# Performance work log

Hardware: AMD Instinct MI355X
Metric: run time of the kernel (lower is better)

The kernel has to match this reference:

```python
import jax, jax.numpy as jnp
import numpy as np
import math

H = 1024      # hidden_size
NH = 16       # num_attention_heads
HD = H // NH  # head_dim = 64
FF = 4096     # intermediate_size
AD = 256      # adapter_hidden_size
NB = 320      # num_buckets
MAXD = 800    # max_bucket_distance
B = 4
S = 1024
EPS = 1e-5


def _rel_bucket(rel):
    # HF WavLM _relative_positions_bucket
    nb = NB // 2
    buckets = (rel > 0).astype(jnp.int32) * nb
    rel = jnp.abs(rel)
    max_exact = nb // 2
    is_small = rel < max_exact
    large = max_exact + (
        jnp.log(jnp.maximum(rel, 1).astype(jnp.float32) / max_exact)
        / math.log(MAXD / max_exact) * (nb - max_exact)
    ).astype(jnp.int32)
    large = jnp.minimum(large, nb - 1)
    return buckets + jnp.where(is_small, rel, large)


def _ln(x, g, b):
    m = x.mean(-1, keepdims=True)
    v = ((x - m) ** 2).mean(-1, keepdims=True)
    return (x - m) * jax.lax.rsqrt(v + EPS) * g + b


def setup_inputs() -> dict:
    key = jax.random.key(0)
    ks = jax.random.split(key, 12)
    sc = 0.02
    w = lambda k, shape: jax.random.normal(k, shape, jnp.float32) * sc
    return dict(
        x=jax.random.normal(ks[0], (B, S, H), jnp.float32),
        Wq=w(ks[1], (H, H)), bq=jnp.zeros((H,), jnp.float32),
        Wk=w(ks[2], (H, H)), bk=jnp.zeros((H,), jnp.float32),
        Wv=w(ks[3], (H, H)), bv=jnp.zeros((H,), jnp.float32),
        Wo=w(ks[4], (H, H)), bo=jnp.zeros((H,), jnp.float32),
        Wg=w(ks[5], (8, HD)), bg=jnp.zeros((8,), jnp.float32),
        gru_const=jnp.ones((1, NH, 1, 1), jnp.float32),
        rel_embed=w(ks[6], (NB, NH)),
        ln1_g=jnp.ones((H,), jnp.float32), ln1_b=jnp.zeros((H,), jnp.float32),
        W1=w(ks[7], (FF, H)), b1=jnp.zeros((FF,), jnp.float32),
        W2=w(ks[8], (H, FF)), b2=jnp.zeros((H,), jnp.float32),
        ln2_g=jnp.ones((H,), jnp.float32), ln2_b=jnp.zeros((H,), jnp.float32),
        Wad=w(ks[9], (AD, H)), bad=jnp.zeros((AD,), jnp.float32),
        Wau=w(ks[10], (H, AD)), bau=jnp.zeros((H,), jnp.float32),
    )


def reference(x, Wq, bq, Wk, bk, Wv, bv, Wo, bo, Wg, bg, gru_const, rel_embed,
              ln1_g, ln1_b, W1, b1, W2, b2, ln2_g, ln2_b, Wad, bad, Wau, bau):
    b, s, _ = x.shape
    # --- relative position bias (first layer: position_bias=None) ---
    pos = jnp.arange(s)
    rel = pos[None, :] - pos[:, None]                 # memory - context
    pos_bias = rel_embed[_rel_bucket(rel)].transpose(2, 0, 1)  # (nh, s, s)

    # --- GRU-style gating of the bias (per batch, head, query pos) ---
    xh = x.reshape(b, s, NH, HD).transpose(0, 2, 1, 3)         # (b, nh, s, hd)
    gproj = jnp.einsum('bhsd,ed->bhse', xh, Wg) + bg           # (b, nh, s, 8)
    gproj = gproj.reshape(b, NH, s, 2, 4).sum(-1)              # (b, nh, s, 2)
    gate = jax.nn.sigmoid(gproj)
    gate_a, gate_b = gate[..., 0:1], gate[..., 1:2]            # (b, nh, s, 1)
    gate_out = gate_a * (gate_b * gru_const - 1.0) + 2.0       # (b, nh, s, 1)
    gated_bias = gate_out * pos_bias[None]                     # (b, nh, s, s)

    # --- multi-head self-attention with additive gated bias ---
    q = (x @ Wq.T + bq).reshape(b, s, NH, HD)
    k = (x @ Wk.T + bk).reshape(b, s, NH, HD)
    v = (x @ Wv.T + bv).reshape(b, s, NH, HD)
    scores = jnp.einsum('bihd,bjhd->bhij', q, k) * (HD ** -0.5) + gated_bias
    attn = jax.nn.softmax(scores, axis=-1)
    ctx = jnp.einsum('bhij,bjhd->bihd', attn, v).reshape(b, s, H)
    attn_out = ctx @ Wo.T + bo

    # --- residual + LN, FFN + adapter (idx_without_adapter=None path) + LN ---
    h = _ln(x + attn_out, ln1_g, ln1_b)
    ff = jax.nn.gelu(h @ W1.T + b1, approximate=False) @ W2.T + b2
    adapt = jax.nn.elu(h @ Wad.T + bad) @ Wau.T + bau
    h = h + ff + adapt
    return _ln(h, ln2_g, ln2_b)
```

## Files before the change

### kernel.cpp

```cpp
#include <hip/hip_runtime.h>
#include <cmath>

typedef unsigned short u16;
using short8 = __attribute__((ext_vector_type(8))) short;
using f32x4  = __attribute__((ext_vector_type(4))) float;

__device__ __forceinline__ u16 f2bf(float f) {
  union { float f; unsigned u; } c; c.f = f;
  unsigned r = c.u + 0x7fffu + ((c.u >> 16) & 1u);
  return (u16)(r >> 16);
}
__device__ __forceinline__ float bf2f(u16 b) {
  union { unsigned u; float f; } c; c.u = ((unsigned)b) << 16;
  return c.f;
}

__device__ __forceinline__ void gld_lds16(void* lds, const void* g) {
  __builtin_amdgcn_global_load_lds(
      (const __attribute__((address_space(1))) void*)g,
      (__attribute__((address_space(3))) void*)lds, 16, 0, 0);
}

__device__ __forceinline__ float gelu_fast(float t) {
  float u = 0.7978845608f * t * (1.f + 0.044715f * t * t);
  float th = 1.f - 2.f / (__expf(2.f * u) + 1.f);
  return 0.5f * t * (1.f + th);
}

__global__ __launch_bounds__(256) void cvt_bf16(const float* __restrict__ in,
                                                u16* __restrict__ out, int n4) {
  int i = blockIdx.x * 256 + threadIdx.x;
  if (i >= n4) return;
  float4 v = ((const float4*)in)[i];
  ushort4 o;
  o.x = f2bf(v.x); o.y = f2bf(v.y); o.z = f2bf(v.z); o.w = f2bf(v.w);
  ((ushort4*)out)[i] = o;
}

__global__ __launch_bounds__(256) void cvt_pad(const float* __restrict__ in,
                                               u16* __restrict__ out,
                                               int incols4, int outstride, int n4) {
  int i = blockIdx.x * 256 + threadIdx.x;
  if (i >= n4) return;
  int row = i / incols4, c = i - row * incols4;
  float4 v = ((const float4*)in)[i];
  ushort4 o;
  o.x = f2bf(v.x); o.y = f2bf(v.y); o.z = f2bf(v.z); o.w = f2bf(v.w);
  *(ushort4*)&out[(size_t)row * outstride + c * 4] = o;
}

__global__ __launch_bounds__(256) void btab_kernel(const float* __restrict__ rel_embed,
                                                   float* __restrict__ btab) {
  int idx = blockIdx.x * 256 + threadIdx.x;
  if (idx >= 16 * 2048) return;
  int h = idx >> 11;
  int d = idx & 2047;
  if (d >= 2047) return;
  int rel = d - 1023;
  int bucket = (rel > 0) ? 160 : 0;
  int ar = rel < 0 ? -rel : rel;
  if (ar < 80) {
    bucket += ar;
  } else {
    int large = 80 + (int)(logf((float)ar / 80.0f) / 2.3025851f * 80.0f);
    if (large > 159) large = 159;
    bucket += large;
  }
  btab[h * 2048 + d] = rel_embed[bucket * 16 + h];
}

__global__ __launch_bounds__(256) void gate_kernel(const float* __restrict__ x,
                                                   const float* __restrict__ Wg,
                                                   const float* __restrict__ bg,
                                                   const float* __restrict__ gc,
                                                   float* __restrict__ gate_out) {
  int gw = blockIdx.x * 4 + (threadIdx.x >> 6);
  int lane = threadIdx.x & 63;
  int s = gw & 1023, bh = gw >> 10, b = bh >> 4, h = bh & 15;
  float wA = Wg[lane] + Wg[64 + lane] + Wg[128 + lane] + Wg[192 + lane];
  float wB = Wg[256 + lane] + Wg[320 + lane] + Wg[384 + lane] + Wg[448 + lane];
  float xv = x[((size_t)(b * 1024 + s)) * 1024 + h * 64 + lane];
  float pa = xv * wA, pb = xv * wB;
  #pragma unroll
  for (int m = 1; m < 64; m <<= 1) {
    pa += __shfl_xor(pa, m, 64);
    pb += __shfl_xor(pb, m, 64);
  }
  if (lane == 0) {
    float bgA = bg[0] + bg[1] + bg[2] + bg[3];
    float bgB = bg[4] + bg[5] + bg[6] + bg[7];
    float ga = 1.f / (1.f + expf(-(pa + bgA)));
    float gb = 1.f / (1.f + expf(-(pb + bgB)));
    gate_out[(size_t)bh * 1024 + s] = ga * (gb * gc[h] - 1.f) + 2.f;
  }
}

__global__ __launch_bounds__(256) void vtrans_kernel(const u16* __restrict__ vb,
                                                     u16* __restrict__ vt) {
  __shared__ u16 tile[64 * 65];
  int bh = blockIdx.y, b = bh >> 4, h = bh & 15;
  int s0 = blockIdx.x * 64;
  int tid = threadIdx.x;
  int r = tid >> 3, c = (tid & 7) * 8;
  #pragma unroll
  for (int p = 0; p < 2; ++p) {
    int s = p * 32 + r;
    uint4 vv = *(const uint4*)&vb[((size_t)(b * 1024 + s0 + s)) * 1024 + h * 64 + c];
    const u16* pv = (const u16*)&vv;
    #pragma unroll
    for (int e = 0; e < 8; ++e) tile[(c + e) * 65 + s] = pv[e];
  }
  __syncthreads();
  int d = tid & 63, jc0 = tid >> 6;
  #pragma unroll
  for (int jc = jc0; jc < 8; jc += 4) {
    u16 tmp[8];
    #pragma unroll
    for (int e = 0; e < 8; ++e) tmp[e] = tile[d * 65 + jc * 8 + e];
    *(uint4*)&vt[((size_t)(bh * 64 + d)) * 1024 + s0 + jc * 8] = *(uint4*)tmp;
  }
}

template <int MODE>
__global__ __launch_bounds__(256, 3) void gemm_bt(
    const u16* __restrict__ A, const u16* __restrict__ Bw,
    int K, int Ksub, int N,
    const float* __restrict__ bias0, const float* __restrict__ bias1,
    const float* __restrict__ bias2,
    float* __restrict__ outf,
    u16* __restrict__ ob0, u16* __restrict__ ob1, u16* __restrict__ ob2) {
  __shared__ __align__(16) u16 As[3][128 * 32];
  __shared__ __align__(16) u16 Bs[3][128 * 32];
  const int tid = threadIdx.x;
  const int lane = tid & 63, wave = tid >> 6;
  const int quad = lane >> 4, l16 = lane & 15;
  const int bm = blockIdx.x * 128, bn = blockIdx.y * 128;
  const int kz = blockIdx.z;
  const int nsteps = Ksub >> 5;
  const int wm = (wave & 1) * 64, wn = (wave >> 1) * 64;
  const int sr = lane & 15, skc = (lane >> 4) * 8;

  const u16* a0 = A + (size_t)(bm + wave * 32 + sr) * K + kz * Ksub + skc;
  const u16* b0 = Bw + (size_t)(bn + wave * 32 + sr) * K + kz * Ksub + skc;
  const size_t ra = (size_t)16 * K;

  f32x4 acc[4][4] = {};

  #pragma unroll
  for (int t = 0; t < 2; ++t) {
    gld_lds16(&As[0][(wave * 2 + t) * 512], a0 + t * ra);
    gld_lds16(&Bs[0][(wave * 2 + t) * 512], b0 + t * ra);
  }
  if (nsteps > 1) {
    #pragma unroll
    for (int t = 0; t < 2; ++t) {
      gld_lds16(&As[1][(wave * 2 + t) * 512], a0 + t * ra + 32);
      gld_lds16(&Bs[1][(wave * 2 + t) * 512], b0 + t * ra + 32);
    }
  }

  int cur = 0, nxt2 = 2;
  for (int ks = 0; ks < nsteps; ++ks) {
    if (ks + 1 < nsteps) asm volatile("s_waitcnt vmcnt(4)" ::: "memory");
    else                 asm volatile("s_waitcnt vmcnt(0)" ::: "memory");
    __builtin_amdgcn_s_barrier();
    if (ks + 2 < nsteps) {
      int ko = (ks + 2) * 32;
      #pragma unroll
      for (int t = 0; t < 2; ++t) {
        gld_lds16(&As[nxt2][(wave * 2 + t) * 512], a0 + t * ra + ko);
        gld_lds16(&Bs[nxt2][(wave * 2 + t) * 512], b0 + t * ra + ko);
      }
    }
    const u16* Ap = As[cur];
    const u16* Bp = Bs[cur];
    short8 af[4], bf[4];
    #pragma unroll
    for (int mi = 0; mi < 4; ++mi)
      af[mi] = *(const short8*)&Ap[((wm >> 4) + mi) * 512 + quad * 128 + l16 * 8];
    #pragma unroll
    for (int ni = 0; ni < 4; ++ni)
      bf[ni] = *(const short8*)&Bp[((wn >> 4) + ni) * 512 + quad * 128 + l16 * 8];
    #pragma unroll
    for (int mi = 0; mi < 4; ++mi)
      #pragma unroll
      for (int ni = 0; ni < 4; ++ni)
        acc[mi][ni] = __builtin_amdgcn_mfma_f32_16x16x32_bf16(af[mi], bf[ni], acc[mi][ni], 0, 0, 0);
    cur = (cur == 2) ? 0 : cur + 1;
    nxt2 = (nxt2 == 2) ? 0 : nxt2 + 1;
  }

  float* outp = outf + (size_t)kz * 4194304;

  #pragma unroll
  for (int mi = 0; mi < 4; ++mi) {
    #pragma unroll
    for (int ni = 0; ni < 4; ++ni) {
      int col = bn + wn + ni * 16 + l16;
      #pragma unroll
      for (int r = 0; r < 4; ++r) {
        int m = bm + wm + mi * 16 + quad * 4 + r;
        float v = acc[mi][ni][r];
        if constexpr (MODE == 0) {
          int seg = col >> 10;
          int nloc = col & 1023;
          const float* bs = seg == 0 ? bias0 : (seg == 1 ? bias1 : bias2);
          u16* dst = seg == 0 ? ob0 : (seg == 1 ? ob1 : ob2);
          v += bs[nloc];
          if (seg == 0) v *= 0.125f;
          dst[(size_t)m * 1024 + nloc] = f2bf(v);
        } else if constexpr (MODE == 2) {
          if (col < 4096) {
            float t = v + bias0[col];
            ob0[(size_t)m * 4352 + col] = f2bf(gelu_fast(t));
          } else {
            float t = v + bias1[col - 4096];
            float e = t > 0.f ? t : (__expf(t) - 1.f);
            ob0[(size_t)m * 4352 + col] = f2bf(e);
          }
        } else {
          outp[(size_t)m * N + col] = v;
        }
      }
    }
  }
}

__global__ __launch_bounds__(256) void attn_kernel(
    const u16* __restrict__ qb, const u16* __restrict__ kb, const u16* __restrict__ vt,
    const float* __restrict__ gate, const float* __restrict__ btab,
    u16* __restrict__ ctxb) {
  __shared__ __align__(16) u16 Qs[64 * 64];
  __shared__ __align__(16) u16 Ks[64 * 64];
  __shared__ __align__(16) u16 Vs[64 * 64];
  __shared__ __align__(16) u16 Ps[4][16 * 64];
  __shared__ u16 btl[2048];
  __shared__ float gbuf[64];

  const int tid = threadIdx.x;
  const int lane = tid & 63, wave = tid >> 6;
  const int quad = lane >> 4, l16 = lane & 15;
  const int it0 = blockIdx.x * 64;
  const int bh = blockIdx.y, b = bh >> 4, h = bh & 15;
  const int sr = lane & 15;
  const int skc = (lane >> 4) * 8;

  for (int idx = tid; idx < 2047; idx += 256) btl[idx] = f2bf(btab[h * 2048 + idx]);
  if (tid < 64) gbuf[tid] = gate[(size_t)bh * 1024 + it0 + tid];

  #pragma unroll
  for (int hf = 0; hf < 2; ++hf)
    gld_lds16(&Qs[wave * 1024 + hf * 512],
              &qb[((size_t)(b * 1024 + it0 + wave * 16 + sr)) * 1024 + h * 64 + hf * 32 + skc]);

  f32x4 oacc[4] = {};
  float mrow[4], lrow[4];
  #pragma unroll
  for (int r = 0; r < 4; ++r) { mrow[r] = -1e30f; lrow[r] = 0.f; }

  __syncthreads();

  for (int jt = 0; jt < 16; ++jt) {
    int j0 = jt * 64;
    #pragma unroll
    for (int hf = 0; hf < 2; ++hf) {
      gld_lds16(&Ks[wave * 1024 + hf * 512],
                &kb[((size_t)(b * 1024 + j0 + wave * 16 + sr)) * 1024 + h * 64 + hf * 32 + skc]);
      gld_lds16(&Vs[wave * 1024 + hf * 512],
                &vt[((size_t)(bh * 64 + wave * 16 + sr)) * 1024 + j0 + hf * 32 + skc]);
    }
    __syncthreads();

    f32x4 sacc[4] = {};
    #pragma unroll
    for (int c = 0; c < 2; ++c) {
      short8 aq = *(const short8*)&Qs[wave * 1024 + (c * 4 + quad) * 128 + l16 * 8];
      #pragma unroll
      for (int nt = 0; nt < 4; ++nt) {
        short8 bk8 = *(const short8*)&Ks[nt * 1024 + (c * 4 + quad) * 128 + l16 * 8];
        sacc[nt] = __builtin_amdgcn_mfma_f32_16x16x32_bf16(aq, bk8, sacc[nt], 0, 0, 0);
      }
    }

    float sc[4][4], mt[4];
    #pragma unroll
    for (int r = 0; r < 4; ++r) {
      int i_loc = wave * 16 + quad * 4 + r;
      int i_glob = it0 + i_loc;
      float g = gbuf[i_loc];
      float mx = -1e30f;
      #pragma unroll
      for (int nt = 0; nt < 4; ++nt) {
        int j = j0 + nt * 16 + l16;
        float s = sacc[nt][r] + g * bf2f(btl[j - i_glob + 1023]);
        sc[nt][r] = s;
        mx = fmaxf(mx, s);
      }
      mt[r] = mx;
    }
    #pragma unroll
    for (int m = 1; m < 16; m <<= 1)
      #pragma unroll
      for (int r = 0; r < 4; ++r) mt[r] = fmaxf(mt[r], __shfl_xor(mt[r], m, 64));

    float alpha[4], ls[4];
    #pragma unroll
    for (int r = 0; r < 4; ++r) {
      float mnew = fmaxf(mrow[r], mt[r]);
      alpha[r] = __expf(mrow[r] - mnew);
      mrow[r] = mnew;
      float lsum = 0.f;
      #pragma unroll
      for (int nt = 0; nt < 4; ++nt) {
        float p = __expf(sc[nt][r] - mnew);
        sc[nt][r] = p;
        lsum += p;
      }
      ls[r] = lsum;
    }
    #pragma unroll
    for (int m = 1; m < 16; m <<= 1)
      #pragma unroll
      for (int r = 0; r < 4; ++r) ls[r] += __shfl_xor(ls[r], m, 64);
    #pragma unroll
    for (int r = 0; r < 4; ++r) lrow[r] = lrow[r] * alpha[r] + ls[r];

    #pragma unroll
    for (int nt = 0; nt < 4; ++nt)
      #pragma unroll
      for (int r = 0; r < 4; ++r)
        Ps[wave][(nt * 2 + (l16 >> 3)) * 128 + (quad * 4 + r) * 8 + (l16 & 7)] = f2bf(sc[nt][r]);

    #pragma unroll
    for (int dt = 0; dt < 4; ++dt)
      #pragma unroll
      for (int r = 0; r < 4; ++r) oacc[dt][r] *= alpha[r];

    #pragma unroll
    for (int c = 0; c < 2; ++c) {
      short8 ap = *(const short8*)&Ps[wave][(c * 4 + quad) * 128 + l16 * 8];
      #pragma unroll
      for (int dt = 0; dt < 4; ++dt) {
        short8 bv8 = *(const short8*)&Vs[dt * 1024 + (c * 4 + quad) * 128 + l16 * 8];
        oacc[dt] = __builtin_amdgcn_mfma_f32_16x16x32_bf16(ap, bv8, oacc[dt], 0, 0, 0);
      }
    }
    __syncthreads();
  }

  #pragma unroll
  for (int dt = 0; dt < 4; ++dt)
    #pragma unroll
    for (int r = 0; r < 4; ++r) {
      int i_loc = wave * 16 + quad * 4 + r;
      int d = dt * 16 + l16;
      float o = oacc[dt][r] / lrow[r];
      ctxb[((size_t)(b * 1024 + it0 + i_loc)) * 1024 + h * 64 + d] = f2bf(o);
    }
}

template <bool WRITE_BF16, bool TWO_BIAS>
__global__ __launch_bounds__(256) void redln_kernel(
    const float* __restrict__ p0, const float* __restrict__ p1,
    const float* __restrict__ extra, const float* __restrict__ bias,
    const float* __restrict__ bias2,
    const float* __restrict__ g, const float* __restrict__ bta,
    float* __restrict__ outf, u16* __restrict__ outb) {
  __shared__ float red[8];
  int row = blockIdx.x, tid = threadIdx.x;
  int lane = tid & 63, wave = tid >> 6;
  size_t base = (size_t)row * 1024 + tid * 4;
  float4 a = *(const float4*)&p0[base];
  float4 bb = *(const float4*)&p1[base];
  float4 c = *(const float4*)&extra[base];
  float4 d = *(const float4*)&bias[tid * 4];
  float4 v;
  v.x = a.x + bb.x + c.x + d.x;
  v.y = a.y + bb.y + c.y + d.y;
  v.z = a.z + bb.z + c.z + d.z;
  v.w = a.w + bb.w + c.w + d.w;
  if (TWO_BIAS) {
    float4 d2 = *(const float4*)&bias2[tid * 4];
    v.x += d2.x; v.y += d2.y; v.z += d2.z; v.w += d2.w;
  }
  float s = v.x + v.y + v.z + v.w;
  #pragma unroll
  for (int m = 1; m < 64; m <<= 1) s += __shfl_xor(s, m, 64);
  if (lane == 0) red[wave] = s;
  __syncthreads();
  float mean = (red[0] + red[1] + red[2] + red[3]) * (1.f / 1024.f);
  float d0 = v.x - mean, d1 = v.y - mean, d2 = v.z - mean, d3 = v.w - mean;
  float sq = d0 * d0 + d1 * d1 + d2 * d2 + d3 * d3;
  #pragma unroll
  for (int m = 1; m < 64; m <<= 1) sq += __shfl_xor(sq, m, 64);
  if (lane == 0) red[4 + wave] = sq;
  __syncthreads();
  float var = (red[4] + red[5] + red[6] + red[7]) * (1.f / 1024.f);
  float rstd = rsqrtf(var + 1e-5f);
  float dd[4] = {d0, d1, d2, d3};
  #pragma unroll
  for (int e = 0; e < 4; ++e) {
    int cidx = tid * 4 + e;
    float val = dd[e] * rstd * g[cidx] + bta[cidx];
    outf[(size_t)row * 1024 + cidx] = val;
    if (WRITE_BF16) outb[(size_t)row * 1024 + cidx] = f2bf(val);
  }
}

extern "C" void kernel_launch(void* const* d_in, const int* in_sizes, int n_in,
                              void* d_out, int out_size, void* d_ws, size_t ws_size,
                              hipStream_t stream) {
  const float* x    = (const float*)d_in[0];
  const float* Wq   = (const float*)d_in[1];  const float* bq  = (const float*)d_in[2];
  const float* Wk   = (const float*)d_in[3];  const float* bk  = (const float*)d_in[4];
  const float* Wv   = (const float*)d_in[5];  const float* bv  = (const float*)d_in[6];
  const float* Wo   = (const float*)d_in[7];  const float* bo  = (const float*)d_in[8];
  const float* Wg   = (const float*)d_in[9];  const float* bg  = (const float*)d_in[10];
  const float* gc   = (const float*)d_in[11];
  const float* rel  = (const float*)d_in[12];
  const float* ln1g = (const float*)d_in[13]; const float* ln1b = (const float*)d_in[14];
  const float* W1   = (const float*)d_in[15]; const float* b1  = (const float*)d_in[16];
  const float* W2   = (const float*)d_in[17]; const float* b2  = (const float*)d_in[18];
  const float* ln2g = (const float*)d_in[19]; const float* ln2b = (const float*)d_in[20];
  const float* Wad  = (const float*)d_in[21]; const float* bad = (const float*)d_in[22];
  const float* Wau  = (const float*)d_in[23]; const float* bau = (const float*)d_in[24];
  float* out = (float*)d_out;

  char* ws = (char*)d_ws;
  const size_t MB = 1ull << 20;
  const size_t KB = 1ull << 10;
  u16*   xb    = (u16*)(ws + 0 * MB);
  u16*   wqkv  = (u16*)(ws + 8 * MB);
  u16*   qb    = (u16*)(ws + 14 * MB);
  u16*   kb    = (u16*)(ws + 22 * MB);
  u16*   vbp   = (u16*)(ws + 30 * MB);
  u16*   vtb   = (u16*)(ws + 38 * MB);
  float* gate  = (float*)(ws + 46 * MB);
  float* btab  = (float*)(ws + 46 * MB + 256 * KB);
  u16*   ffadp = (u16*)(ws + 0 * MB);
  float* P0    = (float*)(ws + 34 * MB);
  float* P1    = (float*)(ws + 50 * MB);
  u16*   ctxb  = (u16*)(ws + 66 * MB);
  u16*   wob   = (u16*)(ws + 74 * MB);
  u16*   w1ad  = (u16*)(ws + 76 * MB);
  u16*   w2au  = (u16*)(ws + 85 * MB);
  float* hf    = (float*)(ws + 94 * MB);
  u16*   hb    = (u16*)(ws + 110 * MB);
  (void)ws_size; (void)n_in; (void)in_sizes; (void)out_size;

  auto cvt = [&](const float* src, u16* dst, int n) {
    cvt_bf16<<<(n / 4 + 255) / 256, 256, 0, stream>>>(src, dst, n / 4);
  };
  cvt(x, xb, 4096 * 1024);
  cvt(Wq, wqkv,               1024 * 1024);
  cvt(Wk, wqkv + 1024 * 1024, 1024 * 1024);
  cvt(Wv, wqkv + 2 * 1024 * 1024, 1024 * 1024);
  cvt(Wo, wob, 1024 * 1024);
  cvt(W1, w1ad, 4096 * 1024);
  cvt(Wad, w1ad + 4096 * 1024, 256 * 1024);
  cvt_pad<<<(1024 * 1024 + 255) / 256, 256, 0, stream>>>(W2, w2au, 1024, 4352, 1024 * 1024);
  cvt_pad<<<(64 * 1024 + 255) / 256, 256, 0, stream>>>(Wau, w2au + 4096, 64, 4352, 64 * 1024);

  btab_kernel<<<128, 256, 0, stream>>>(rel, btab);
  gate_kernel<<<16384, 256, 0, stream>>>(x, Wg, bg, gc, gate);

  gemm_bt<0><<<dim3(32, 24, 1), 256, 0, stream>>>(xb, wqkv, 1024, 1024, 3072,
      bq, bk, bv, nullptr, qb, kb, vbp);
  vtrans_kernel<<<dim3(16, 64), 256, 0, stream>>>(vbp, vtb);
  attn_kernel<<<dim3(16, 64), 256, 0, stream>>>(qb, kb, vtb, gate, btab, ctxb);
  gemm_bt<3><<<dim3(32, 8, 2), 256, 0, stream>>>(ctxb, wob, 1024, 512, 1024,
      nullptr, nullptr, nullptr, P0, nullptr, nullptr, nullptr);
  redln_kernel<true, false><<<4096, 256, 0, stream>>>(P0, P1, x, bo, nullptr,
      ln1g, ln1b, hf, hb);
  gemm_bt<2><<<dim3(32, 34, 1), 256, 0, stream>>>(hb, w1ad, 1024, 1024, 4352,
      b1, bad, nullptr, nullptr, ffadp, nullptr, nullptr);
  gemm_bt<3><<<dim3(32, 8, 2), 256, 0, stream>>>(ffadp, w2au, 4352, 2176, 1024,
      nullptr, nullptr, nullptr, P0, nullptr, nullptr, nullptr);
  redln_kernel<false, true><<<4096, 256, 0, stream>>>(P0, P1, hf, b2, bau,
      ln2g, ln2b, out, nullptr);
}
```

Measured before the change: 538.6 us.

## Add 256x256 double-buffered GEMM kernel with 8-wave pipelining for large projections

Adds a new 512-thread GEMM kernel that computes 256x256 tiles, loads into LDS directly from global memory with swizzled offsets, uses phased barriers with set-priority around the MFMA blocks, and remaps block indices for locality. It replaces the QKV, FFN-up and FFN-down GEMMs. The adapter slice of FFN-up moves to a small launch of the old kernel using a new column offset. When the workspace is large enough, the workspace is laid out again and FFN-down uses a 4-way K split with a 4-input reduce+LN. The larger tiles mean fewer blocks, which risks leaving CUs idle on small grids such as 16x4x2.

```diff
diff --git a/kernel.cpp b/kernel.cpp
--- a/kernel.cpp
+++ b/kernel.cpp
@@ -124,7 +124,7 @@
 template <int MODE>
 __global__ __launch_bounds__(256, 3) void gemm_bt(
     const u16* __restrict__ A, const u16* __restrict__ Bw,
-    int K, int Ksub, int N,
+    int K, int Ksub, int N, int bn0,
     const float* __restrict__ bias0, const float* __restrict__ bias1,
     const float* __restrict__ bias2,
     float* __restrict__ outf,
@@ -196,7 +196,7 @@
   for (int mi = 0; mi < 4; ++mi) {
     #pragma unroll
     for (int ni = 0; ni < 4; ++ni) {
-      int col = bn + wn + ni * 16 + l16;
+      int col = bn + bn0 + wn + ni * 16 + l16;
       #pragma unroll
       for (int r = 0; r < 4; ++r) {
         int m = bm + wm + mi * 16 + quad * 4 + r;
@@ -226,6 +226,170 @@
   }
 }
 
+#define VMCNT(n) asm volatile("s_waitcnt vmcnt(" #n ")" ::: "memory")
+#define NOOPST ((void)0)
+
+#define G256_LDA(BUF, KK, MH)                                               \
+  af_[0] = *(const short8*)&lds[BUF][0][KK][aBase + (MH) * 2048 + 0];       \
+  af_[1] = *(const short8*)&lds[BUF][0][KK][aBase + (MH) * 2048 + 512];     \
+  af_[2] = *(const short8*)&lds[BUF][0][KK][aBase + (MH) * 2048 + 1024];    \
+  af_[3] = *(const short8*)&lds[BUF][0][KK][aBase + (MH) * 2048 + 1536];
+#define G256_LDB(BUF, KK)                                                   \
+  bf_[0] = *(const short8*)&lds[BUF][1][KK][bBase + 0];                     \
+  bf_[1] = *(const short8*)&lds[BUF][1][KK][bBase + 512];                   \
+  bf_[2] = *(const short8*)&lds[BUF][1][KK][bBase + 1024];                  \
+  bf_[3] = *(const short8*)&lds[BUF][1][KK][bBase + 1536];
+#define G256_MFMA(MH)                                                       \
+  _Pragma("unroll") for (int mi = 0; mi < 4; ++mi)                          \
+  _Pragma("unroll") for (int ni = 0; ni < 4; ++ni)                          \
+    acc[(MH) * 4 + mi][ni] = __builtin_amdgcn_mfma_f32_16x16x32_bf16(       \
+        af_[mi], bf_[ni], acc[(MH) * 4 + mi][ni], 0, 0, 0);
+#define G256_PHASE(BUF, KK, MH, DOB, STAGE, WAIT)                           \
+  {                                                                         \
+    G256_LDA(BUF, KK, MH)                                                   \
+    if (DOB) { G256_LDB(BUF, KK) }                                          \
+    STAGE;                                                                  \
+    __builtin_amdgcn_s_barrier();                                           \
+    asm volatile("s_waitcnt lgkmcnt(0)" ::: "memory");                      \
+    __builtin_amdgcn_s_setprio(1);                                          \
+    G256_MFMA(MH)                                                           \
+    __builtin_amdgcn_s_setprio(0);                                          \
+    WAIT;                                                                   \
+    __builtin_amdgcn_s_barrier();                                           \
+  }
+
+template <int MODE>
+__global__ __launch_bounds__(512, 2) void gemm256(
+    const u16* __restrict__ A, const u16* __restrict__ Bw,
+    int lda, int ldb, int kt_hi, int kt_lo, int z_hi,
+    const float* __restrict__ bias0, const float* __restrict__ bias1,
+    const float* __restrict__ bias2,
+    float* __restrict__ outf, float* __restrict__ outf2, int ldo,
+    u16* __restrict__ ob0, u16* __restrict__ ob1, u16* __restrict__ ob2) {
+  __shared__ __align__(16) u16 lds[2][2][2][8192];
+
+  const int tid = threadIdx.x;
+  const int lane = tid & 63, wave = tid >> 6;
+  const int quad = lane >> 4, l16 = lane & 15;
+  const int wm = wave >> 2, wn = wave & 3;
+
+  const int gx = gridDim.x, gy = gridDim.y;
+  int flat = blockIdx.x + gx * (blockIdx.y + gy * blockIdx.z);
+  const int cpx = (gx * gy * gridDim.z) >> 3;
+  flat = (flat & 7) * cpx + (flat >> 3);
+  const int bmi = flat % gx;
+  int rest = flat / gx;
+  const int bni = rest % gy;
+  const int kz = rest / gy;
+
+  const int bm = bmi * 256, bn = bni * 256;
+  const int nkt = (kz < z_hi) ? kt_hi : kt_lo;
+  const int ktb = (kz < z_hi) ? kz * kt_hi : z_hi * kt_hi + (kz - z_hi) * kt_lo;
+  const int nIter = nkt >> 1;
+
+  const int srow = wave * 16 + (lane >> 2);
+  const int sk = (((lane & 3) ^ ((lane >> 3) & 3)) << 3);
+  const u16* aG = A + (size_t)(bm + srow) * lda + (size_t)ktb * 64 + sk;
+  const u16* bG = Bw + (size_t)(bn + srow) * ldb + (size_t)ktb * 64 + sk;
+  const size_t aS = (size_t)128 * lda, bS = (size_t)128 * ldb;
+
+  const int xsw = ((quad ^ ((l16 >> 1) & 3)) << 3);
+  const int aBase = (wm * 128 + l16) * 32 + xsw;
+  const int bBase = (wn * 64 + l16) * 32 + xsw;
+
+  auto stA = [&](int buf, int kh, int kt) {
+    const u16* g = aG + kt * 64 + kh * 32;
+    u16* d = (u16*)&lds[buf][0][kh][wave * 512];
+    gld_lds16(d, g);
+    gld_lds16(d + 4096, g + aS);
+  };
+  auto stB = [&](int buf, int kh, int kt) {
+    const u16* g = bG + kt * 64 + kh * 32;
+    u16* d = (u16*)&lds[buf][1][kh][wave * 512];
+    gld_lds16(d, g);
+    gld_lds16(d + 4096, g + bS);
+  };
+
+  f32x4 acc[8][4] = {};
+  short8 af_[4], bf_[4];
+
+  stA(0, 0, 0); stB(0, 0, 0); stA(0, 1, 0); stB(0, 1, 0);
+  stA(1, 0, 1); stB(1, 0, 1);
+  VMCNT(0);
+  __builtin_amdgcn_s_barrier();
+
+  for (int J = 0; J < nIter - 1; ++J) {
+    const int o = 2 * J + 1, e = 2 * J + 2, on = 2 * J + 3;
+    G256_PHASE(0, 0, 0, 1, stA(1, 1, o),  NOOPST)
+    G256_PHASE(0, 0, 1, 0, stB(1, 1, o),  VMCNT(8))
+    G256_PHASE(0, 1, 0, 1, stA(0, 0, e),  NOOPST)
+    G256_PHASE(0, 1, 1, 0, stB(0, 0, e),  VMCNT(8))
+    G256_PHASE(1, 0, 0, 1, stA(0, 1, e),  NOOPST)
+    G256_PHASE(1, 0, 1, 0, stB(0, 1, e),  VMCNT(8))
+    G256_PHASE(1, 1, 0, 1, stA(1, 0, on), NOOPST)
+    G256_PHASE(1, 1, 1, 0, stB(1, 0, on), VMCNT(8))
+  }
+  {
+    const int o = nkt - 1;
+    G256_PHASE(0, 0, 0, 1, stA(1, 1, o), NOOPST)
+    G256_PHASE(0, 0, 1, 0, stB(1, 1, o), NOOPST)
+    G256_PHASE(0, 1, 0, 1, NOOPST,       NOOPST)
+    G256_PHASE(0, 1, 1, 0, NOOPST,       VMCNT(4))
+    G256_PHASE(1, 0, 0, 1, NOOPST,       NOOPST)
+    G256_PHASE(1, 0, 1, 0, NOOPST,       VMCNT(0))
+    G256_PHASE(1, 1, 0, 1, NOOPST,       NOOPST)
+    G256_PHASE(1, 1, 1, 0, NOOPST,       NOOPST)
+  }
+
+  const int m0 = bm + wm * 128 + quad * 4;
+  const int n0 = bn + wn * 64 + l16;
+
+  if constexpr (MODE == 0) {
+    const int seg = bn >> 10;
+    const float* bs = seg == 0 ? bias0 : (seg == 1 ? bias1 : bias2);
+    u16* dst = seg == 0 ? ob0 : (seg == 1 ? ob1 : ob2);
+    const float sc = seg == 0 ? 0.125f : 1.0f;
+    const int nb = (bn & 1023) + wn * 64 + l16;
+    #pragma unroll
+    for (int a = 0; a < 8; ++a)
+      #pragma unroll
+      for (int ni = 0; ni < 4; ++ni) {
+        int nn = nb + ni * 16;
+        float bv = bs[nn];
+        #pragma unroll
+        for (int r = 0; r < 4; ++r) {
+          int m = m0 + a * 16 + r;
+          dst[(size_t)m * 1024 + nn] = f2bf((acc[a][ni][r] + bv) * sc);
+        }
+      }
+  } else if constexpr (MODE == 2) {
+    #pragma unroll
+    for (int a = 0; a < 8; ++a)
+      #pragma unroll
+      for (int ni = 0; ni < 4; ++ni) {
+        int nn = n0 + ni * 16;
+        float bv = bias0[nn];
+        #pragma unroll
+        for (int r = 0; r < 4; ++r) {
+          int m = m0 + a * 16 + r;
+          ob0[(size_t)m * 4352 + nn] = f2bf(gelu_fast(acc[a][ni][r] + bv));
+        }
+      }
+  } else {
+    float* op = (kz < 2) ? outf + (size_t)kz * 4194304
+                         : outf2 + (size_t)(kz - 2) * 4194304;
+    #pragma unroll
+    for (int a = 0; a < 8; ++a)
+      #pragma unroll
+      for (int ni = 0; ni < 4; ++ni) {
+        int nn = n0 + ni * 16;
+        #pragma unroll
+        for (int r = 0; r < 4; ++r)
+          op[(size_t)(m0 + a * 16 + r) * ldo + nn] = acc[a][ni][r];
+      }
+  }
+}
+
 __global__ __launch_bounds__(256) void attn_kernel(
     const u16* __restrict__ qb, const u16* __restrict__ kb, const u16* __restrict__ vt,
     const float* __restrict__ gate, const float* __restrict__ btab,
@@ -359,9 +523,10 @@
     }
 }
 
-template <bool WRITE_BF16, bool TWO_BIAS>
+template <bool WRITE_BF16, bool TWO_BIAS, int NP>
 __global__ __launch_bounds__(256) void redln_kernel(
     const float* __restrict__ p0, const float* __restrict__ p1,
+    const float* __restrict__ p2, const float* __restrict__ p3,
     const float* __restrict__ extra, const float* __restrict__ bias,
     const float* __restrict__ bias2,
     const float* __restrict__ g, const float* __restrict__ bta,
@@ -379,6 +544,12 @@
   v.y = a.y + bb.y + c.y + d.y;
   v.z = a.z + bb.z + c.z + d.z;
   v.w = a.w + bb.w + c.w + d.w;
+  if (NP == 4) {
+    float4 e2 = *(const float4*)&p2[base];
+    float4 e3 = *(const float4*)&p3[base];
+    v.x += e2.x + e3.x; v.y += e2.y + e3.y;
+    v.z += e2.z + e3.z; v.w += e2.w + e3.w;
+  }
   if (TWO_BIAS) {
     float4 d2 = *(const float4*)&bias2[tid * 4];
     v.x += d2.x; v.y += d2.y; v.z += d2.z; v.w += d2.w;
@@ -429,24 +600,47 @@
   char* ws = (char*)d_ws;
   const size_t MB = 1ull << 20;
   const size_t KB = 1ull << 10;
-  u16*   xb    = (u16*)(ws + 0 * MB);
-  u16*   wqkv  = (u16*)(ws + 8 * MB);
-  u16*   qb    = (u16*)(ws + 14 * MB);
-  u16*   kb    = (u16*)(ws + 22 * MB);
-  u16*   vbp   = (u16*)(ws + 30 * MB);
-  u16*   vtb   = (u16*)(ws + 38 * MB);
-  float* gate  = (float*)(ws + 46 * MB);
-  float* btab  = (float*)(ws + 46 * MB + 256 * KB);
-  u16*   ffadp = (u16*)(ws + 0 * MB);
-  float* P0    = (float*)(ws + 34 * MB);
-  float* P1    = (float*)(ws + 50 * MB);
-  u16*   ctxb  = (u16*)(ws + 66 * MB);
-  u16*   wob   = (u16*)(ws + 74 * MB);
-  u16*   w1ad  = (u16*)(ws + 76 * MB);
-  u16*   w2au  = (u16*)(ws + 85 * MB);
-  float* hf    = (float*)(ws + 94 * MB);
-  u16*   hb    = (u16*)(ws + 110 * MB);
-  (void)ws_size; (void)n_in; (void)in_sizes; (void)out_size;
+  (void)n_in; (void)in_sizes; (void)out_size;
+
+  const bool big = ws_size >= (135ull << 20);
+
+  u16 *xb, *wqkv, *qb, *kb, *vbp, *vtb, *ctxb, *wob, *w1ad, *w2au, *ffadp, *hb;
+  float *gate, *btab, *P0, *P1, *P2, *P3, *hf;
+  xb    = (u16*)(ws + 0 * MB);
+  wqkv  = (u16*)(ws + 8 * MB);
+  ffadp = (u16*)(ws + 0 * MB);
+  P0    = (float*)(ws + 34 * MB);
+  P1    = (float*)(ws + 50 * MB);
+  if (big) {
+    P2   = (float*)(ws + 66 * MB);
+    P3   = (float*)(ws + 82 * MB);
+    qb   = (u16*)(ws + 66 * MB);
+    kb   = (u16*)(ws + 74 * MB);
+    vbp  = (u16*)(ws + 82 * MB);
+    vtb  = (u16*)(ws + 90 * MB);
+    hb   = (u16*)(ws + 82 * MB);
+    ctxb = (u16*)(ws + 98 * MB);
+    hf   = (float*)(ws + 98 * MB);
+    wob  = (u16*)(ws + 114 * MB);
+    w1ad = (u16*)(ws + 116 * MB);
+    w2au = (u16*)(ws + 125 * MB);
+    gate = (float*)(ws + 133 * MB + 512 * KB);
+    btab = (float*)(ws + 133 * MB + 768 * KB);
+  } else {
+    P2   = P0;  P3 = P0;
+    qb   = (u16*)(ws + 14 * MB);
+    kb   = (u16*)(ws + 22 * MB);
+    vbp  = (u16*)(ws + 30 * MB);
+    vtb  = (u16*)(ws + 38 * MB);
+    gate = (float*)(ws + 46 * MB);
+    btab = (float*)(ws + 46 * MB + 256 * KB);
+    ctxb = (u16*)(ws + 66 * MB);
+    wob  = (u16*)(ws + 74 * MB);
+    w1ad = (u16*)(ws + 76 * MB);
+    w2au = (u16*)(ws + 85 * MB);
+    hf   = (float*)(ws + 94 * MB);
+    hb   = (u16*)(ws + 110 * MB);
+  }
 
   auto cvt = [&](const float* src, u16* dst, int n) {
     cvt_bf16<<<(n / 4 + 255) / 256, 256, 0, stream>>>(src, dst, n / 4);
@@ -464,18 +658,27 @@
   btab_kernel<<<128, 256, 0, stream>>>(rel, btab);
   gate_kernel<<<16384, 256, 0, stream>>>(x, Wg, bg, gc, gate);
 
-  gemm_bt<0><<<dim3(32, 24, 1), 256, 0, stream>>>(xb, wqkv, 1024, 1024, 3072,
-      bq, bk, bv, nullptr, qb, kb, vbp);
+  gemm256<0><<<dim3(16, 12, 1), 512, 0, stream>>>(xb, wqkv, 1024, 1024, 16, 16, 1,
+      bq, bk, bv, nullptr, nullptr, 0, qb, kb, vbp);
   vtrans_kernel<<<dim3(16, 64), 256, 0, stream>>>(vbp, vtb);
   attn_kernel<<<dim3(16, 64), 256, 0, stream>>>(qb, kb, vtb, gate, btab, ctxb);
-  gemm_bt<3><<<dim3(32, 8, 2), 256, 0, stream>>>(ctxb, wob, 1024, 512, 1024,
+  gemm_bt<3><<<dim3(32, 8, 2), 256, 0, stream>>>(ctxb, wob, 1024, 512, 1024, 0,
       nullptr, nullptr, nullptr, P0, nullptr, nullptr, nullptr);
-  redln_kernel<true, false><<<4096, 256, 0, stream>>>(P0, P1, x, bo, nullptr,
+  redln_kernel<true, false, 2><<<4096, 256, 0, stream>>>(P0, P1, P0, P0, x, bo, nullptr,
       ln1g, ln1b, hf, hb);
-  gemm_bt<2><<<dim3(32, 34, 1), 256, 0, stream>>>(hb, w1ad, 1024, 1024, 4352,
-      b1, bad, nullptr, nullptr, ffadp, nullptr, nullptr);
-  gemm_bt<3><<<dim3(32, 8, 2), 256, 0, stream>>>(ffadp, w2au, 4352, 2176, 1024,
-      nullptr, nullptr, nullptr, P0, nullptr, nullptr, nullptr);
-  redln_kernel<false, true><<<4096, 256, 0, stream>>>(P0, P1, hf, b2, bau,
-      ln2g, ln2b, out, nullptr);
-}
+  gemm256<2><<<dim3(16, 16, 1), 512, 0, stream>>>(hb, w1ad, 1024, 1024, 16, 16, 1,
+      b1, nullptr, nullptr, nullptr, nullptr, 0, ffadp, nullptr, nullptr);
+  gemm_bt<2><<<dim3(32, 2, 1), 256, 0, stream>>>(hb, w1ad + 4096 * 1024, 1024, 1024, 4352,
+      4096, bad, bad, nullptr, nullptr, ffadp, nullptr, nullptr);
+  if (big) {
+    gemm256<3><<<dim3(16, 4, 4), 512, 0, stream>>>(ffadp, w2au, 4352, 4352, 18, 16, 2,
+        nullptr, nullptr, nullptr, P0, P2, 1024, nullptr, nullptr, nullptr);
+    redln_kernel<false, true, 4><<<4096, 256, 0, stream>>>(P0, P1, P2, P3, hf, b2, bau,
+        ln2g, ln2b, out, nullptr);
+  } else {
+    gemm256<3><<<dim3(16, 4, 2), 512, 0, stream>>>(ffadp, w2au, 4352, 4352, 34, 34, 2,
+        nullptr, nullptr, nullptr, P0, P2, 1024, nullptr, nullptr, nullptr);
+    redln_kernel<false, true, 2><<<4096, 256, 0, stream>>>(P0, P1, P0, P0, hf, b2, bau,
+        ln2g, ln2b, out, nullptr);
+  }
+}
```

Result: no change. 548.8 us (+1.9%).
